# Optimization experiments

Hardware: AMD Instinct MI355X
Metric: run time of the kernel (lower is better)

## Reference

```python
import jax, jax.numpy as jnp
import numpy as np

N_NODES = 100000
N_EDGES = 600000
N_GRAPHS = 4096
F_IN = 74
H = 128
L = 3
BN_EPS = 1e-5


def setup_inputs() -> dict:
    key = jax.random.key(0)
    ks = jax.random.split(key, 12)
    x = jax.random.normal(ks[0], (N_NODES, F_IN), dtype=jnp.float32)
    edge_index = jax.random.randint(ks[1], (2, N_EDGES), 0, N_NODES)
    batch = jnp.sort(jax.random.randint(ks[2], (N_NODES,), 0, N_GRAPHS))

    def lin(k, fan_in, fan_out):
        return (jax.random.normal(k, (fan_in, fan_out), dtype=jnp.float32)
                / np.float32(np.sqrt(fan_in)))

    emb_W = lin(ks[3], F_IN, H)
    emb_b = jnp.zeros((H,), jnp.float32)
    conv_W = jax.random.normal(ks[4], (L, H, H), dtype=jnp.float32) / np.float32(np.sqrt(H))
    conv_b = jnp.zeros((L, H), jnp.float32)
    bn_gamma = jnp.ones((L, H), jnp.float32)
    bn_beta = jnp.zeros((L, H), jnp.float32)
    w1 = lin(ks[5], 2 * H, H)
    b1 = jnp.zeros((H,), jnp.float32)
    w2 = lin(ks[6], H, H // 2)
    b2 = jnp.zeros((H // 2,), jnp.float32)
    w3 = lin(ks[7], H // 2, 1)
    b3 = jnp.zeros((1,), jnp.float32)
    return dict(x=x, edge_index=edge_index, batch=batch,
                emb_W=emb_W, emb_b=emb_b, conv_W=conv_W, conv_b=conv_b,
                bn_gamma=bn_gamma, bn_beta=bn_beta,
                w1=w1, b1=b1, w2=w2, b2=b2, w3=w3, b3=b3)


def reference(x, edge_index, batch, emb_W, emb_b, conv_W, conv_b,
              bn_gamma, bn_beta, w1, b1, w2, b2, w3, b3):
    N = x.shape[0]
    # GCN normalization with self-loops (PyG GCNConv semantics)
    loops = jnp.arange(N)
    src = jnp.concatenate([edge_index[0], loops])  # [E+N]
    dst = jnp.concatenate([edge_index[1], loops])
    deg = jax.ops.segment_sum(jnp.ones_like(dst, jnp.float32), dst, num_segments=N)
    dinv = jax.lax.rsqrt(jnp.maximum(deg, 1.0))  # deg >= 1 due to self-loops
    norm = dinv[src] * dinv[dst]                 # [E+N]

    h = jax.nn.relu(x @ emb_W + emb_b)           # [N, H]
    for i in range(L):
        hw = h @ conv_W[i]                       # [N, H]
        msg = hw[src] * norm[:, None]            # gather + scale  [E+N, H]
        h = jax.ops.segment_sum(msg, dst, num_segments=N) + conv_b[i]
        # BatchNorm1d, training-mode batch statistics (biased variance)
        mu = jnp.mean(h, axis=0)
        var = jnp.mean((h - mu) ** 2, axis=0)
        h = (h - mu) * jax.lax.rsqrt(var + BN_EPS) * bn_gamma[i] + bn_beta[i]
        h = jax.nn.relu(h)
        # dropout: identity (inference / deterministic baseline)

    # segment mean / max pooling over graphs
    cnt = jax.ops.segment_sum(jnp.ones((N,), jnp.float32), batch, num_segments=N_GRAPHS)
    g_mean = jax.ops.segment_sum(h, batch, num_segments=N_GRAPHS) / jnp.maximum(cnt, 1.0)[:, None]
    g_max = jax.ops.segment_max(h, batch, num_segments=N_GRAPHS)
    g_max = jnp.where(jnp.isfinite(g_max), g_max, 0.0)  # guard empty segments
    g = jnp.concatenate([g_mean, g_max], axis=1)         # [G, 2H]

    h1 = jax.nn.relu(g @ w1 + b1)
    h2 = jax.nn.relu(h1 @ w2 + b2)
    return h2 @ w3 + b3                                   # [G, 1]
```

## Files before the change

### kernel.cpp

```cpp
#include <hip/hip_runtime.h>

#define NN 100000
#define NE 600000
#define NG 4096
#define FIN 74
#define HD 128
#define NL 3
#define BN_EPS 1e-5f
#define NSCAN 391
#define NHISTB 2344
#define NTILES 3125
#define NSHADOW 8

typedef __attribute__((ext_vector_type(8))) short short8;
typedef __attribute__((ext_vector_type(4))) float floatx4;
typedef __attribute__((ext_vector_type(8))) unsigned short bf16x8;
typedef __attribute__((ext_vector_type(4))) unsigned short bf16x4;

__device__ __forceinline__ unsigned short f2bf(float f) {
    unsigned u = __float_as_uint(f);
    u += 0x7fff + ((u >> 16) & 1);
    return (unsigned short)(u >> 16);
}
__device__ __forceinline__ float bf2f(unsigned short u) {
    return __uint_as_float(((unsigned)u) << 16);
}

__global__ __launch_bounds__(256) void k_pre(const int* __restrict__ dst,
                                             int* __restrict__ degi,
                                             const int* __restrict__ batch,
                                             int* __restrict__ gstart,
                                             const float* __restrict__ embW,
                                             const float* __restrict__ convW,
                                             unsigned short* __restrict__ WfE,
                                             unsigned short* __restrict__ WfC) {
    int blk = blockIdx.x;
    int t = threadIdx.x;
    if (blk < NHISTB) {
        int e = blk * 256 + t;
        if (e < NE) atomicAdd(&degi[dst[e]], 1);
    } else if (blk < NHISTB + NSCAN) {
        int n = (blk - NHISTB) * 256 + t;
        if (n >= NN) return;
        int b = batch[n];
        int bp = (n == 0) ? -1 : batch[n - 1];
        for (int g = bp + 1; g <= b; g++) gstart[g] = n;
        if (n == NN - 1)
            for (int g = b + 1; g <= NG; g++) gstart[g] = NN;
    } else {
        int d = (blk - NHISTB - NSCAN) * 256 + t;
        if (d < 12288) {
            int inner = d & 511, outer = d >> 9;
            int kstep = outer % 3, nt = outer / 3;
            int g = inner >> 7, n = (inner >> 3) & 15, j = inner & 7;
            int k = kstep * 32 + g * 8 + j;
            float v = (k < FIN) ? embW[k * HD + nt * 16 + n] : 0.0f;
            WfE[d] = f2bf(v);
        } else {
            int e = d - 12288;
            if (e >= NL * 16384) return;
            int layer = e >> 14, r = e & 16383;
            int j = r & 7, n = (r >> 3) & 15, g = (r >> 7) & 3, kstep = (r >> 9) & 3, nt = r >> 11;
            int k = kstep * 32 + g * 8 + j;
            WfC[e] = f2bf(convW[layer * 16384 + k * HD + nt * 16 + n]);
        }
    }
}

__global__ __launch_bounds__(256) void k_scan1(const int* __restrict__ degi,
                                               int* __restrict__ part) {
    __shared__ int s[256];
    int t = threadIdx.x;
    int idx = blockIdx.x * 256 + t;
    s[t] = (idx < NN) ? degi[idx] : 0;
    __syncthreads();
    for (int off = 128; off > 0; off >>= 1) {
        if (t < off) s[t] += s[t + off];
        __syncthreads();
    }
    if (t == 0) part[blockIdx.x] = s[0];
}

__global__ __launch_bounds__(512) void k_scan2(int* __restrict__ part) {
    __shared__ int s[512];
    int t = threadIdx.x;
    s[t] = (t < NSCAN) ? part[t] : 0;
    __syncthreads();
    for (int off = 1; off < 512; off <<= 1) {
        int v = s[t];
        int a = (t >= off) ? s[t - off] : 0;
        __syncthreads();
        s[t] = v + a;
        __syncthreads();
    }
    if (t < NSCAN) part[t] = (t > 0) ? s[t - 1] : 0;
}

__global__ __launch_bounds__(256) void k_scan3(const int* __restrict__ degi,
                                               const int* __restrict__ part,
                                               int* __restrict__ rowptr,
                                               float* __restrict__ dinv) {
    __shared__ int s[256];
    int t = threadIdx.x;
    int idx = blockIdx.x * 256 + t;
    int v = (idx < NN) ? degi[idx] : 0;
    s[t] = v;
    __syncthreads();
    for (int off = 1; off < 256; off <<= 1) {
        int x = s[t];
        int a = (t >= off) ? s[t - off] : 0;
        __syncthreads();
        s[t] = x + a;
        __syncthreads();
    }
    if (idx < NN) {
        rowptr[idx] = part[blockIdx.x] + (s[t] - v);
        dinv[idx] = rsqrtf((float)v + 1.0f);
    }
    if (idx == 0) rowptr[NN] = NE;
}

__global__ __launch_bounds__(256) void k_fill(const int* __restrict__ src,
                                              const int* __restrict__ dst,
                                              const int* __restrict__ rowptr,
                                              int* __restrict__ cursor,
                                              int* __restrict__ col) {
    int e = blockIdx.x * 256 + threadIdx.x;
    if (e >= NE) return;
    int d = dst[e];
    int pos = rowptr[d] + atomicAdd(&cursor[d], 1);
    col[pos] = src[e];
}

__global__ __launch_bounds__(256) void k_emb(const float* __restrict__ x,
                                             const unsigned short* __restrict__ Wf,
                                             const float* __restrict__ b,
                                             unsigned short* __restrict__ hA) {
    __shared__ __align__(16) unsigned short As[4224];
    int t = threadIdx.x;
    int n0 = blockIdx.x * 32;
    for (int f = t; f < 3072; f += 256) {
        int m = f / 96, kp = f % 96;
        float v = (kp < FIN) ? x[(n0 + m) * FIN + kp] : 0.0f;
        int kstep = kp >> 5, g = (kp >> 3) & 3, j = kp & 7;
        As[(kstep * 4 + g) * 264 + m * 8 + j] = f2bf(v);
    }
    __syncthreads();
    int lane = t & 63, wv = t >> 6;
    int lanelo = lane & 15, g = lane >> 4;
    floatx4 acc[2][2] = {};
#pragma unroll
    for (int kstep = 0; kstep < 3; kstep++) {
        short8 a0 = *(const short8*)&As[(kstep * 4 + g) * 264 + lanelo * 8];
        short8 a1 = *(const short8*)&As[(kstep * 4 + g) * 264 + 128 + lanelo * 8];
        short8 b0 = *(const short8*)&Wf[(((wv * 2 + 0) * 3 + kstep) * 4 + g) * 128 + lanelo * 8];
        short8 b1 = *(const short8*)&Wf[(((wv * 2 + 1) * 3 + kstep) * 4 + g) * 128 + lanelo * 8];
        acc[0][0] = __builtin_amdgcn_mfma_f32_16x16x32_bf16(a0, b0, acc[0][0], 0, 0, 0);
        acc[0][1] = __builtin_amdgcn_mfma_f32_16x16x32_bf16(a0, b1, acc[0][1], 0, 0, 0);
        acc[1][0] = __builtin_amdgcn_mfma_f32_16x16x32_bf16(a1, b0, acc[1][0], 0, 0, 0);
        acc[1][1] = __builtin_amdgcn_mfma_f32_16x16x32_bf16(a1, b1, acc[1][1], 0, 0, 0);
    }
    __syncthreads();
#pragma unroll
    for (int ns = 0; ns < 2; ns++) {
        int colc = wv * 32 + ns * 16 + lanelo;
        float bias = b[colc];
#pragma unroll
        for (int ms = 0; ms < 2; ms++)
#pragma unroll
            for (int r = 0; r < 4; r++) {
                int rowl = ms * 16 + g * 4 + r;
                As[rowl * 132 + colc] = f2bf(fmaxf(acc[ms][ns][r] + bias, 0.0f));
            }
    }
    __syncthreads();
#pragma unroll
    for (int i = 0; i < 2; i++) {
        int f = t * 8 + i * 2048;
        int m = f >> 7, c = f & 127;
        bf16x4 lo = *(const bf16x4*)&As[m * 132 + c];
        bf16x4 hi = *(const bf16x4*)&As[m * 132 + c + 4];
        bf16x8 o = {lo.x, lo.y, lo.z, lo.w, hi.x, hi.y, hi.z, hi.w};
        *(bf16x8*)&hA[n0 * HD + f] = o;
    }
}

template <bool BN>
__global__ __launch_bounds__(256) void k_fused(const unsigned short* __restrict__ Ain,
                                               const int* __restrict__ rowptr,
                                               const int* __restrict__ col,
                                               const float* __restrict__ dinv,
                                               const float* __restrict__ bnprev,
                                               const float* __restrict__ gamma,
                                               const float* __restrict__ beta,
                                               const unsigned short* __restrict__ Wf,
                                               const float* __restrict__ bias,
                                               float* __restrict__ bnout,
                                               unsigned short* __restrict__ Aout) {
    __shared__ __align__(16) unsigned short As[4224];
    int t = threadIdx.x;
    int sub = t >> 4;
    int lanec = t & 15;
    int k0 = lanec * 8;

    float sc[8], sh[8];
    if (BN) {
        const float inv_n = 1.0f / (float)NN;
#pragma unroll
        for (int jj = 0; jj < 8; jj++) {
            int c = k0 + jj;
            float s = 0.0f, q = 0.0f;
#pragma unroll
            for (int kk = 0; kk < NSHADOW; kk++) {
                s += bnprev[kk * 256 + c];
                q += bnprev[kk * 256 + 128 + c];
            }
            float mu = s * inv_n;
            float var = q * inv_n - mu * mu;
            float g = gamma[c] * rsqrtf(var + BN_EPS);
            sc[jj] = g;
            sh[jj] = beta[c] - mu * g;
        }
    }

    int lane = t & 63, wv = t >> 6;
    int lanelo = lane & 15, g = lane >> 4;
    float bias0 = bias[wv * 32 + lanelo];
    float bias1 = bias[wv * 32 + 16 + lanelo];
    float ssum[2] = {}, ssq[2] = {};

    int n0 = blockIdx.x * 32;
#pragma unroll
    for (int p = 0; p < 2; p++) {
        int n = n0 + p * 16 + sub;
        float dn = dinv[n];
        float acc[8];
        bf16x8 u = *(const bf16x8*)&Ain[n * HD + k0];
#pragma unroll
        for (int i = 0; i < 8; i++) {
            float v = bf2f(u[i]);
            if (BN) v = fmaxf(v * sc[i] + sh[i], 0.0f);
            acc[i] = dn * v;
        }
        int j = rowptr[n], j1 = rowptr[n + 1];
        for (; j + 3 < j1; j += 4) {
            int s0 = col[j], s1 = col[j + 1], s2 = col[j + 2], s3 = col[j + 3];
            float d0 = dinv[s0], d1 = dinv[s1], d2 = dinv[s2], d3 = dinv[s3];
            bf16x8 v0 = *(const bf16x8*)&Ain[s0 * HD + k0];
            bf16x8 v1 = *(const bf16x8*)&Ain[s1 * HD + k0];
            bf16x8 v2 = *(const bf16x8*)&Ain[s2 * HD + k0];
            bf16x8 v3 = *(const bf16x8*)&Ain[s3 * HD + k0];
#pragma unroll
            for (int i = 0; i < 8; i++) {
                float a0 = bf2f(v0[i]);
                float a1 = bf2f(v1[i]);
                float a2 = bf2f(v2[i]);
                float a3 = bf2f(v3[i]);
                if (BN) {
                    a0 = fmaxf(a0 * sc[i] + sh[i], 0.0f);
                    a1 = fmaxf(a1 * sc[i] + sh[i], 0.0f);
                    a2 = fmaxf(a2 * sc[i] + sh[i], 0.0f);
                    a3 = fmaxf(a3 * sc[i] + sh[i], 0.0f);
                }
                acc[i] = fmaf(d0, a0, acc[i]);
                acc[i] = fmaf(d1, a1, acc[i]);
                acc[i] = fmaf(d2, a2, acc[i]);
                acc[i] = fmaf(d3, a3, acc[i]);
            }
        }
        for (; j < j1; j++) {
            int s0 = col[j];
            float d0 = dinv[s0];
            bf16x8 v0 = *(const bf16x8*)&Ain[s0 * HD + k0];
#pragma unroll
            for (int i = 0; i < 8; i++) {
                float a = bf2f(v0[i]);
                if (BN) a = fmaxf(a * sc[i] + sh[i], 0.0f);
                acc[i] = fmaf(d0, a, acc[i]);
            }
        }
        bf16x8 o;
#pragma unroll
        for (int i = 0; i < 8; i++) o[i] = f2bf(acc[i] * dn);
        *(bf16x8*)&As[lanec * 264 + (p * 16 + sub) * 8] = o;
    }
    __syncthreads();
    floatx4 macc[2][2] = {};
#pragma unroll
    for (int ks = 0; ks < 4; ks++) {
        short8 a0 = *(const short8*)&As[(ks * 4 + g) * 264 + lanelo * 8];
        short8 a1 = *(const short8*)&As[(ks * 4 + g) * 264 + 128 + lanelo * 8];
        short8 b0 = *(const short8*)&Wf[(((wv * 2 + 0) * 4 + ks) * 4 + g) * 128 + lanelo * 8];
        short8 b1 = *(const short8*)&Wf[(((wv * 2 + 1) * 4 + ks) * 4 + g) * 128 + lanelo * 8];
        macc[0][0] = __builtin_amdgcn_mfma_f32_16x16x32_bf16(a0, b0, macc[0][0], 0, 0, 0);
        macc[0][1] = __builtin_amdgcn_mfma_f32_16x16x32_bf16(a0, b1, macc[0][1], 0, 0, 0);
        macc[1][0] = __builtin_amdgcn_mfma_f32_16x16x32_bf16(a1, b0, macc[1][0], 0, 0, 0);
        macc[1][1] = __builtin_amdgcn_mfma_f32_16x16x32_bf16(a1, b1, macc[1][1], 0, 0, 0);
    }
    __syncthreads();
#pragma unroll
    for (int ms = 0; ms < 2; ms++)
#pragma unroll
        for (int ns = 0; ns < 2; ns++) {
            int colc = wv * 32 + ns * 16 + lanelo;
            float bb = ns ? bias1 : bias0;
#pragma unroll
            for (int r = 0; r < 4; r++) {
                int rowl = ms * 16 + g * 4 + r;
                float v = macc[ms][ns][r] + bb;
                ssum[ns] += v;
                ssq[ns] += v * v;
                As[rowl * 132 + colc] = f2bf(v);
            }
        }
    __syncthreads();
#pragma unroll
    for (int i = 0; i < 2; i++) {
        int f = t * 8 + i * 2048;
        int m = f >> 7, c = f & 127;
        bf16x4 lo = *(const bf16x4*)&As[m * 132 + c];
        bf16x4 hi = *(const bf16x4*)&As[m * 132 + c + 4];
        bf16x8 o = {lo.x, lo.y, lo.z, lo.w, hi.x, hi.y, hi.z, hi.w};
        *(bf16x8*)&Aout[n0 * HD + f] = o;
    }
    __syncthreads();
    float* ls = (float*)As;
    ls[t] = 0.0f;
    __syncthreads();
    {
        int colc0 = wv * 32 + lanelo;
        atomicAdd(&ls[colc0], ssum[0]);
        atomicAdd(&ls[128 + colc0], ssq[0]);
        atomicAdd(&ls[colc0 + 16], ssum[1]);
        atomicAdd(&ls[128 + colc0 + 16], ssq[1]);
    }
    __syncthreads();
    atomicAdd(&bnout[(blockIdx.x & (NSHADOW - 1)) * 256 + t], ls[t]);
}

__global__ __launch_bounds__(128) void k_pool_g(const unsigned short* __restrict__ h,
                                                const float* __restrict__ bnsum,
                                                const float* __restrict__ gamma,
                                                const float* __restrict__ beta,
                                                const int* __restrict__ gstart,
                                                float* __restrict__ gfeat) {
    int g = blockIdx.x;
    int c = threadIdx.x;
    int n0 = gstart[g], n1 = gstart[g + 1];
    const float inv_n = 1.0f / (float)NN;
    float s0 = 0.0f, q0 = 0.0f;
#pragma unroll
    for (int k = 0; k < NSHADOW; k++) {
        s0 += bnsum[k * 256 + c];
        q0 += bnsum[k * 256 + 128 + c];
    }
    float mu = s0 * inv_n;
    float var = q0 * inv_n - mu * mu;
    float sc = gamma[c] * rsqrtf(var + BN_EPS);
    float sh = beta[c] - mu * sc;
    float s = 0.0f, mx = 0.0f;
    for (int n = n0; n < n1; n++) {
        float v = fmaxf(bf2f(h[n * HD + c]) * sc + sh, 0.0f);
        s += v;
        mx = fmaxf(mx, v);
    }
    float cntf = (float)(n1 - n0);
    gfeat[g * 256 + c] = s / fmaxf(cntf, 1.0f);
    gfeat[g * 256 + HD + c] = mx;
}

__global__ __launch_bounds__(256) void k_mlp(const float* __restrict__ gfeat,
                                             const float* __restrict__ w1,
                                             const float* __restrict__ b1,
                                             const float* __restrict__ w2,
                                             const float* __restrict__ b2,
                                             const float* __restrict__ w3,
                                             const float* __restrict__ b3,
                                             float* __restrict__ out) {
    __shared__ float gs[8][258];
    __shared__ float p1[8][130];
    __shared__ float hs[8][130];
    __shared__ float p2[3][8][66];
    __shared__ float h2s[8][66];
    __shared__ float ps[64];
    int t = threadIdx.x;
    int g0 = blockIdx.x * 8;
    for (int f = t; f < 2048; f += 256) {
        int gi = f >> 8, k = f & 255;
        gs[gi][k] = gfeat[(g0 + gi) * 256 + k];
    }
    __syncthreads();
    {
        int colc = t & 127, half = t >> 7;
        int kb = half * 128;
        float acc[8] = {};
        for (int k = 0; k < 128; k++) {
            float w = w1[(kb + k) * HD + colc];
#pragma unroll
            for (int gi = 0; gi < 8; gi++) acc[gi] += gs[gi][kb + k] * w;
        }
        if (half == 1) {
#pragma unroll
            for (int gi = 0; gi < 8; gi++) p1[gi][colc] = acc[gi];
        }
        __syncthreads();
        if (half == 0) {
            float bias = b1[colc];
#pragma unroll
            for (int gi = 0; gi < 8; gi++)
                hs[gi][colc] = fmaxf(acc[gi] + p1[gi][colc] + bias, 0.0f);
        }
    }
    __syncthreads();
    {
        int colc = t & 63, q = t >> 6;
        int kb = q * 32;
        float acc[8] = {};
        for (int k = 0; k < 32; k++) {
            float w = w2[(kb + k) * 64 + colc];
#pragma unroll
            for (int gi = 0; gi < 8; gi++) acc[gi] += hs[gi][kb + k] * w;
        }
        if (q > 0) {
#pragma unroll
            for (int gi = 0; gi < 8; gi++) p2[q - 1][gi][colc] = acc[gi];
        }
        __syncthreads();
        if (q == 0) {
            float bias = b2[colc];
#pragma unroll
            for (int gi = 0; gi < 8; gi++)
                h2s[gi][colc] = fmaxf(acc[gi] + p2[0][gi][colc] + p2[1][gi][colc]
                                      + p2[2][gi][colc] + bias, 0.0f);
        }
    }
    __syncthreads();
    if (t < 64) {
        int gi = t >> 3, prt = t & 7;
        float p = 0.0f;
#pragma unroll
        for (int k = 0; k < 8; k++) p += h2s[gi][prt * 8 + k] * w3[prt * 8 + k];
        ps[t] = p;
    }
    __syncthreads();
    if (t < 8) {
        float a = b3[0];
#pragma unroll
        for (int i = 0; i < 8; i++) a += ps[t * 8 + i];
        out[g0 + t] = a;
    }
}

extern "C" void kernel_launch(void* const* d_in, const int* in_sizes, int n_in,
                              void* d_out, int out_size, void* d_ws, size_t ws_size,
                              hipStream_t stream) {
    const float* x      = (const float*)d_in[0];
    const int*   eidx   = (const int*)d_in[1];
    const int*   batch  = (const int*)d_in[2];
    const float* emb_W  = (const float*)d_in[3];
    const float* emb_b  = (const float*)d_in[4];
    const float* conv_W = (const float*)d_in[5];
    const float* conv_b = (const float*)d_in[6];
    const float* gamma  = (const float*)d_in[7];
    const float* beta   = (const float*)d_in[8];
    const float* w1     = (const float*)d_in[9];
    const float* b1     = (const float*)d_in[10];
    const float* w2     = (const float*)d_in[11];
    const float* b2     = (const float*)d_in[12];
    const float* w3     = (const float*)d_in[13];
    const float* b3     = (const float*)d_in[14];
    float* out = (float*)d_out;

    const int* src = eidx;
    const int* dst = eidx + NE;

    unsigned short* A = (unsigned short*)d_ws;
    unsigned short* B = A + NN * HD;
    float* dinv  = (float*)(B + NN * HD);
    float* gfeat = dinv + NN;
    float* bnsum3= gfeat + NG * 256;
    int*   degi  = (int*)(bnsum3 + NL * NSHADOW * 256);
    int*   cursor= degi + NN;
    int*   gstart= cursor + NN;
    int*   rowptr= gstart + NG + 1;
    int*   part  = rowptr + NN + 1;
    int*   col   = part + NSCAN;
    unsigned short* WfE = (unsigned short*)(col + NE);
    unsigned short* WfC = WfE + 12288;

    (void)hipMemsetAsync(bnsum3, 0,
                         (NL * NSHADOW * 256) * sizeof(float) + 2 * NN * sizeof(int),
                         stream);
    k_pre<<<NHISTB + NSCAN + 240, 256, 0, stream>>>(dst, degi, batch, gstart,
                                                    emb_W, conv_W, WfE, WfC);
    k_scan1<<<NSCAN, 256, 0, stream>>>(degi, part);
    k_scan2<<<1, 512, 0, stream>>>(part);
    k_scan3<<<NSCAN, 256, 0, stream>>>(degi, part, rowptr, dinv);
    k_fill<<<(NE + 255) / 256, 256, 0, stream>>>(src, dst, rowptr, cursor, col);

    k_emb<<<NN / 32, 256, 0, stream>>>(x, WfE, emb_b, A);

    k_fused<false><<<NTILES, 256, 0, stream>>>(A, rowptr, col, dinv,
                                               nullptr, nullptr, nullptr,
                                               WfC, conv_b, bnsum3, B);
    k_fused<true><<<NTILES, 256, 0, stream>>>(B, rowptr, col, dinv,
                                              bnsum3, gamma, beta,
                                              WfC + 16384, conv_b + HD,
                                              bnsum3 + NSHADOW * 256, A);
    k_fused<true><<<NTILES, 256, 0, stream>>>(A, rowptr, col, dinv,
                                              bnsum3 + NSHADOW * 256,
                                              gamma + HD, beta + HD,
                                              WfC + 2 * 16384, conv_b + 2 * HD,
                                              bnsum3 + 2 * NSHADOW * 256, B);

    k_pool_g<<<NG, 128, 0, stream>>>(B, bnsum3 + 2 * NSHADOW * 256,
                                     gamma + 2 * HD, beta + 2 * HD,
                                     gstart, gfeat);

    k_mlp<<<NG / 8, 256, 0, stream>>>(gfeat, w1, b1, w2, b2, w3, b3, out);
}
```

Measured before the change: 381.4 us.

## Pre-apply BN, ReLU and source dinv scaling in a separate pass before aggregation

The source-side dinv scaling and the BatchNorm+ReLU of the previous layer move out of the gather loop. They are applied once per node, in the embedding epilogue and in a new k_bnact pass that writes pre-scaled features. The gather then becomes plain bf16 additions, with no per-edge dinv loads and no per-edge BN arithmetic, which removes about six-fold redundant work. In exchange it adds two extra full read/write passes over the node features and extra launches, and changes bf16 rounding because dinv is applied before quantization. Launch bounds also gain an occupancy hint of 8.

```diff
diff --git a/kernel.cpp b/kernel.cpp
--- a/kernel.cpp
+++ b/kernel.cpp
@@ -135,10 +135,13 @@
 __global__ __launch_bounds__(256) void k_emb(const float* __restrict__ x,
                                              const unsigned short* __restrict__ Wf,
                                              const float* __restrict__ b,
+                                             const float* __restrict__ dinv,
                                              unsigned short* __restrict__ hA) {
     __shared__ __align__(16) unsigned short As[4224];
+    __shared__ float dinvs[32];
     int t = threadIdx.x;
     int n0 = blockIdx.x * 32;
+    if (t < 32) dinvs[t] = dinv[n0 + t];
     for (int f = t; f < 3072; f += 256) {
         int m = f / 96, kp = f % 96;
         float v = (kp < FIN) ? x[(n0 + m) * FIN + kp] : 0.0f;
@@ -170,7 +173,7 @@
 #pragma unroll
             for (int r = 0; r < 4; r++) {
                 int rowl = ms * 16 + g * 4 + r;
-                As[rowl * 132 + colc] = f2bf(fmaxf(acc[ms][ns][r] + bias, 0.0f));
+                As[rowl * 132 + colc] = f2bf(dinvs[rowl] * fmaxf(acc[ms][ns][r] + bias, 0.0f));
             }
     }
     __syncthreads();
@@ -185,43 +188,55 @@
     }
 }
 
-template <bool BN>
-__global__ __launch_bounds__(256) void k_fused(const unsigned short* __restrict__ Ain,
-                                               const int* __restrict__ rowptr,
-                                               const int* __restrict__ col,
-                                               const float* __restrict__ dinv,
-                                               const float* __restrict__ bnprev,
+__global__ __launch_bounds__(256) void k_bnact(const unsigned short* __restrict__ hpre,
+                                               const float* __restrict__ bnsum,
                                                const float* __restrict__ gamma,
                                                const float* __restrict__ beta,
-                                               const unsigned short* __restrict__ Wf,
-                                               const float* __restrict__ bias,
-                                               float* __restrict__ bnout,
-                                               unsigned short* __restrict__ Aout) {
+                                               const float* __restrict__ dinv,
+                                               unsigned short* __restrict__ P) {
+    int t = threadIdx.x;
+    int cg = t & 15, c0 = cg * 8;
+    const float inv_n = 1.0f / (float)NN;
+    float sc[8], sh[8];
+#pragma unroll
+    for (int jj = 0; jj < 8; jj++) {
+        int c = c0 + jj;
+        float s = 0.0f, q = 0.0f;
+#pragma unroll
+        for (int kk = 0; kk < NSHADOW; kk++) {
+            s += bnsum[kk * 256 + c];
+            q += bnsum[kk * 256 + 128 + c];
+        }
+        float mu = s * inv_n;
+        float var = q * inv_n - mu * mu;
+        float g = gamma[c] * rsqrtf(var + BN_EPS);
+        sc[jj] = g;
+        sh[jj] = beta[c] - mu * g;
+    }
+    for (int n = blockIdx.x * 16 + (t >> 4); n < NN; n += gridDim.x * 16) {
+        float d = dinv[n];
+        bf16x8 u = *(const bf16x8*)&hpre[n * HD + c0];
+        bf16x8 o;
+#pragma unroll
+        for (int i = 0; i < 8; i++)
+            o[i] = f2bf(d * fmaxf(bf2f(u[i]) * sc[i] + sh[i], 0.0f));
+        *(bf16x8*)&P[n * HD + c0] = o;
+    }
+}
+
+__global__ __launch_bounds__(256, 8) void k_fused(const unsigned short* __restrict__ Ain,
+                                                  const int* __restrict__ rowptr,
+                                                  const int* __restrict__ col,
+                                                  const float* __restrict__ dinv,
+                                                  const unsigned short* __restrict__ Wf,
+                                                  const float* __restrict__ bias,
+                                                  float* __restrict__ bnout,
+                                                  unsigned short* __restrict__ Aout) {
     __shared__ __align__(16) unsigned short As[4224];
     int t = threadIdx.x;
     int sub = t >> 4;
     int lanec = t & 15;
     int k0 = lanec * 8;
-
-    float sc[8], sh[8];
-    if (BN) {
-        const float inv_n = 1.0f / (float)NN;
-#pragma unroll
-        for (int jj = 0; jj < 8; jj++) {
-            int c = k0 + jj;
-            float s = 0.0f, q = 0.0f;
-#pragma unroll
-            for (int kk = 0; kk < NSHADOW; kk++) {
-                s += bnprev[kk * 256 + c];
-                q += bnprev[kk * 256 + 128 + c];
-            }
-            float mu = s * inv_n;
-            float var = q * inv_n - mu * mu;
-            float g = gamma[c] * rsqrtf(var + BN_EPS);
-            sc[jj] = g;
-            sh[jj] = beta[c] - mu * g;
-        }
-    }
 
     int lane = t & 63, wv = t >> 6;
     int lanelo = lane & 15, g = lane >> 4;
@@ -237,47 +252,26 @@
         float acc[8];
         bf16x8 u = *(const bf16x8*)&Ain[n * HD + k0];
 #pragma unroll
-        for (int i = 0; i < 8; i++) {
-            float v = bf2f(u[i]);
-            if (BN) v = fmaxf(v * sc[i] + sh[i], 0.0f);
-            acc[i] = dn * v;
-        }
+        for (int i = 0; i < 8; i++) acc[i] = bf2f(u[i]);
         int j = rowptr[n], j1 = rowptr[n + 1];
         for (; j + 3 < j1; j += 4) {
             int s0 = col[j], s1 = col[j + 1], s2 = col[j + 2], s3 = col[j + 3];
-            float d0 = dinv[s0], d1 = dinv[s1], d2 = dinv[s2], d3 = dinv[s3];
             bf16x8 v0 = *(const bf16x8*)&Ain[s0 * HD + k0];
             bf16x8 v1 = *(const bf16x8*)&Ain[s1 * HD + k0];
             bf16x8 v2 = *(const bf16x8*)&Ain[s2 * HD + k0];
             bf16x8 v3 = *(const bf16x8*)&Ain[s3 * HD + k0];
 #pragma unroll
             for (int i = 0; i < 8; i++) {
-                float a0 = bf2f(v0[i]);
-                float a1 = bf2f(v1[i]);
-                float a2 = bf2f(v2[i]);
-                float a3 = bf2f(v3[i]);
-                if (BN) {
-                    a0 = fmaxf(a0 * sc[i] + sh[i], 0.0f);
-                    a1 = fmaxf(a1 * sc[i] + sh[i], 0.0f);
-                    a2 = fmaxf(a2 * sc[i] + sh[i], 0.0f);
-                    a3 = fmaxf(a3 * sc[i] + sh[i], 0.0f);
-                }
-                acc[i] = fmaf(d0, a0, acc[i]);
-                acc[i] = fmaf(d1, a1, acc[i]);
-                acc[i] = fmaf(d2, a2, acc[i]);
-                acc[i] = fmaf(d3, a3, acc[i]);
+                float a01 = bf2f(v0[i]) + bf2f(v1[i]);
+                float a23 = bf2f(v2[i]) + bf2f(v3[i]);
+                acc[i] += a01 + a23;
             }
         }
         for (; j < j1; j++) {
             int s0 = col[j];
-            float d0 = dinv[s0];
             bf16x8 v0 = *(const bf16x8*)&Ain[s0 * HD + k0];
 #pragma unroll
-            for (int i = 0; i < 8; i++) {
-                float a = bf2f(v0[i]);
-                if (BN) a = fmaxf(a * sc[i] + sh[i], 0.0f);
-                acc[i] = fmaf(d0, a, acc[i]);
-            }
+            for (int i = 0; i < 8; i++) acc[i] += bf2f(v0[i]);
         }
         bf16x8 o;
 #pragma unroll
@@ -498,20 +492,19 @@
     k_scan3<<<NSCAN, 256, 0, stream>>>(degi, part, rowptr, dinv);
     k_fill<<<(NE + 255) / 256, 256, 0, stream>>>(src, dst, rowptr, cursor, col);
 
-    k_emb<<<NN / 32, 256, 0, stream>>>(x, WfE, emb_b, A);
-
-    k_fused<false><<<NTILES, 256, 0, stream>>>(A, rowptr, col, dinv,
-                                               nullptr, nullptr, nullptr,
-                                               WfC, conv_b, bnsum3, B);
-    k_fused<true><<<NTILES, 256, 0, stream>>>(B, rowptr, col, dinv,
-                                              bnsum3, gamma, beta,
-                                              WfC + 16384, conv_b + HD,
-                                              bnsum3 + NSHADOW * 256, A);
-    k_fused<true><<<NTILES, 256, 0, stream>>>(A, rowptr, col, dinv,
-                                              bnsum3 + NSHADOW * 256,
-                                              gamma + HD, beta + HD,
-                                              WfC + 2 * 16384, conv_b + 2 * HD,
-                                              bnsum3 + 2 * NSHADOW * 256, B);
+    k_emb<<<NN / 32, 256, 0, stream>>>(x, WfE, emb_b, dinv, A);
+
+    k_fused<<<NTILES, 256, 0, stream>>>(A, rowptr, col, dinv,
+                                        WfC, conv_b, bnsum3, B);
+    k_bnact<<<1024, 256, 0, stream>>>(B, bnsum3, gamma, beta, dinv, A);
+    k_fused<<<NTILES, 256, 0, stream>>>(A, rowptr, col, dinv,
+                                        WfC + 16384, conv_b + HD,
+                                        bnsum3 + NSHADOW * 256, B);
+    k_bnact<<<1024, 256, 0, stream>>>(B, bnsum3 + NSHADOW * 256,
+                                      gamma + HD, beta + HD, dinv, A);
+    k_fused<<<NTILES, 256, 0, stream>>>(A, rowptr, col, dinv,
+                                        WfC + 2 * 16384, conv_b + 2 * HD,
+                                        bnsum3 + 2 * NSHADOW * 256, B);
 
     k_pool_g<<<NG, 128, 0, stream>>>(B, bnsum3 + 2 * NSHADOW * 256,
                                      gamma + 2 * HD, beta + 2 * HD,
```

After: 355.8 us. -6.7%, faster.
